# Kernel optimization log

Hardware: AMD Instinct MI355X
Metric: run time of the kernel (lower is better)

## Reference

```python
import jax, jax.numpy as jnp
import numpy as np
import math

H, B, T = 4, 32, 1000
EPROJS, DUNITS, DK, DV = 1024, 1024, 512, 512
ACONV_CHANS, ACONV_FILTS = 100, 100
FILTS = [ACONV_FILTS * (h + 1) // H for h in range(H)]  # 25, 50, 75, 100


def setup_inputs() -> dict:
    key = jax.random.key(0)
    ks = jax.random.split(key, 16)
    s = 0.02  # small init to keep tanh unsaturated
    ap = jax.random.uniform(ks[3], (H, B, T), dtype=jnp.float32)
    ap = ap / ap.sum(-1, keepdims=True)  # previous attention weights (rows sum to 1)
    inp = {
        "enc_hs_pad": jax.random.normal(ks[0], (B, T, EPROJS), dtype=jnp.float32),
        "enc_hs_len": jnp.full((B,), T, dtype=jnp.int32),
        "dec_z": jax.random.normal(ks[1], (B, DUNITS), dtype=jnp.float32),
        "att_prev": ap,
        "Wq": jax.random.normal(ks[4], (H, DUNITS, DK), dtype=jnp.float32) * s,
        "bq": jnp.zeros((H, DK), dtype=jnp.float32),
        "Wk": jax.random.normal(ks[5], (H, EPROJS, DK), dtype=jnp.float32) * s,
        "Wv": jax.random.normal(ks[6], (H, EPROJS, DV), dtype=jnp.float32) * s,
        "g_w": jax.random.normal(ks[7], (H, DK), dtype=jnp.float32) * s,
        "g_b": jnp.zeros((H,), dtype=jnp.float32),
        "Watt": jax.random.normal(ks[8], (H, ACONV_CHANS, DK), dtype=jnp.float32) * s,
        "Wo": jax.random.normal(ks[9], (H * DV, EPROJS), dtype=jnp.float32) * s,
    }
    for h in range(H):
        inp[f"conv_w{h}"] = jax.random.normal(ks[10 + h], (ACONV_CHANS, 1, 2 * FILTS[h] + 1), dtype=jnp.float32) * s
    return inp


def _conv1d(x, w, f):
    # x: [B, T], w: [C, 1, K]; SAME padding like torch Conv2d(padding=(0, f)) -> [B, C, T]
    return jax.lax.conv_general_dilated(x[:, None, :], w, (1,), [(f, f)],
                                        dimension_numbers=("NCH", "OIH", "NCH"))


def reference(enc_hs_pad, enc_hs_len, dec_z, att_prev, Wq, bq, Wk, Wv, g_w, g_b,
              Watt, Wo, conv_w0, conv_w1, conv_w2, conv_w3):
    scaling = 1.0 / math.sqrt(DK)
    conv_ws = [conv_w0, conv_w1, conv_w2, conv_w3]
    # per-head K/V projections of encoder states: [H, B, T, dk/dv]
    k = jnp.einsum('btd,hde->hbte', enc_hs_pad, Wk)
    v = jnp.einsum('btd,hde->hbte', enc_hs_pad, Wv)
    # per-head query projection: [H, B, dk]
    q = jnp.einsum('bd,hde->hbe', dec_z, Wq) + bq[:, None, :]
    # location features: per-head conv (different filter widths) then linear -> [H, B, T, dk]
    att_conv = jnp.stack([_conv1d(att_prev[h], conv_ws[h], FILTS[h]).transpose(0, 2, 1)
                          for h in range(H)])  # [H, B, T, C]
    att_conv = jnp.einsum('hbtc,hce->hbte', att_conv, Watt)
    # energies via gvec: [H, B, T]
    e = jnp.einsum('hbte,he->hbt', jnp.tanh(k + att_conv + q[:, :, None, :]), g_w) + g_b[:, None, None]
    w = jax.nn.softmax(scaling * e, axis=-1)  # no length masking, as in the original
    # weighted sums per head, concatenated head-major: [B, H*dv]
    c = jnp.einsum('hbte,hbt->bhe', v, w).reshape(B, H * DV)
    out = c @ Wo  # [B, eprojs]
    return out, w
```

## Files before the change

### kernel.cpp

```cpp
#include <hip/hip_runtime.h>
#include <hip/hip_bf16.h>
#include <math.h>

#define Hh 4
#define Bb 32
#define Tt 1000
#define TP 1024
#define EPROJS_ 1024
#define DUNITS_ 1024
#define DKd 512
#define DVd 512
#define CC 100
#define KPAD 256
#define SCALING 0.04419417382415922f

typedef __attribute__((ext_vector_type(8))) short short8;
typedef __attribute__((ext_vector_type(4))) float floatx4;

__device__ __forceinline__ void async16(const void* g, void* l) {
    __builtin_amdgcn_global_load_lds(
        (const __attribute__((address_space(1))) unsigned int*)g,
        (__attribute__((address_space(3))) unsigned int*)l, 16, 0, 0);
}

__device__ __forceinline__ float fast_tanh(float x) {
    float xc = fminf(fmaxf(x, -10.f), 10.f);
    float t = __expf(2.f * xc);
    return (t - 1.f) * __builtin_amdgcn_rcpf(t + 1.f);
}

__global__ __launch_bounds__(256) void enc_cvt_kernel(
    const float* __restrict__ enc, unsigned short* __restrict__ enc16)
{
    int t = blockIdx.x, b = blockIdx.y;
    int d = threadIdx.x * 4;
    float4 v = *(const float4*)(enc + ((size_t)(b * Tt + t)) * EPROJS_ + d);
    union { __hip_bfloat162 h2[2]; uint2 u; } u;
    u.h2[0] = __float22bfloat162_rn(make_float2(v.x, v.y));
    u.h2[1] = __float22bfloat162_rn(make_float2(v.z, v.w));
    *(uint2*)(enc16 + ((size_t)(b * TP + t)) * EPROJS_ + d) = u.u;
}

__global__ __launch_bounds__(256) void wkt_kernel(
    const float* __restrict__ Wk, unsigned short* __restrict__ Wkt)
{
    int et = blockIdx.x;
    int dt = blockIdx.y;
    int h  = blockIdx.z;
    __shared__ float tile[64][65];
    int tid = threadIdx.x;
    int r = tid >> 4, c4 = tid & 15;
    const float* src = Wk + ((size_t)(h * DUNITS_ + dt * 64)) * DKd + et * 64;
#pragma unroll
    for (int rr = 0; rr < 4; ++rr) {
        int row = r + rr * 16;
        *(float4*)&tile[row][c4 * 4] = *(const float4*)(src + (size_t)row * DKd + c4 * 4);
    }
    __syncthreads();
    unsigned short* dst = Wkt + ((size_t)(h * DKd + et * 64)) * EPROJS_ + dt * 64;
#pragma unroll
    for (int rr = 0; rr < 4; ++rr) {
        int el = r + rr * 16;
        union { __hip_bfloat162 h2[2]; uint2 u; } u;
        u.h2[0] = __float22bfloat162_rn(make_float2(tile[c4 * 4 + 0][el], tile[c4 * 4 + 1][el]));
        u.h2[1] = __float22bfloat162_rn(make_float2(tile[c4 * 4 + 2][el], tile[c4 * 4 + 3][el]));
        *(uint2*)(dst + (size_t)el * EPROJS_ + c4 * 4) = u.u;
    }
}

__global__ __launch_bounds__(256) void ww_kernel(
    const float* __restrict__ w0, const float* __restrict__ w1,
    const float* __restrict__ w2, const float* __restrict__ w3,
    const float* __restrict__ Watt, __hip_bfloat16* __restrict__ WWt)
{
    int k = blockIdx.x;
    int h = blockIdx.y;
    int f = 25 * (h + 1), Kh = 2 * f + 1;
    const float* cw = (h == 0) ? w0 : (h == 1) ? w1 : (h == 2) ? w2 : w3;
    int e = threadIdx.x;
    float acc0 = 0.f, acc1 = 0.f;
    if (k < Kh) {
        for (int c = 0; c < CC; ++c) {
            float wv = cw[c * Kh + k];
            acc0 += wv * Watt[(h * CC + c) * DKd + e];
            acc1 += wv * Watt[(h * CC + c) * DKd + e + 256];
        }
    }
    WWt[((size_t)(h * DKd + e)) * KPAD + k] = __float2bfloat16(acc0);
    WWt[((size_t)(h * DKd + e + 256)) * KPAD + k] = __float2bfloat16(acc1);
}

__global__ __launch_bounds__(256) void q_kernel(
    const float* __restrict__ dec_z, const float* __restrict__ Wq,
    float* __restrict__ q_buf)
{
    int et = blockIdx.x, kc = blockIdx.y, h = blockIdx.z;
    int d0 = kc * 64;
    __shared__ float zs[32][64];
    int tid = threadIdx.x;
    {
        int b = tid >> 3, dc = (tid & 7) * 8;
        const float* p = dec_z + (size_t)b * DUNITS_ + d0 + dc;
        *(float4*)&zs[b][dc] = *(const float4*)p;
        *(float4*)&zs[b][dc + 4] = *(const float4*)(p + 4);
    }
    __syncthreads();
    int e = et * 128 + (tid & 127);
    int dl0 = (tid >> 7) * 32;
    float wq[32];
#pragma unroll
    for (int dl = 0; dl < 32; ++dl)
        wq[dl] = Wq[((size_t)(h * DUNITS_ + d0 + dl0 + dl)) * DKd + e];
#pragma unroll
    for (int b = 0; b < 32; ++b) {
        float s = 0.f;
#pragma unroll
        for (int dl = 0; dl < 32; ++dl) s += zs[b][dl0 + dl] * wq[dl];
        atomicAdd(&q_buf[(h * Bb + b) * DKd + e], s);
    }
}

__global__ __launch_bounds__(512, 2) void e_kernel(
    const unsigned short* __restrict__ enc16, const unsigned short* __restrict__ Wkt,
    const float* __restrict__ att_prev, const __hip_bfloat16* __restrict__ WWt,
    const float* __restrict__ q_buf, const float* __restrict__ bq,
    const float* __restrict__ g_w, float* __restrict__ e_buf)
{
    const int lin = blockIdx.x;
    const int xcd = lin & 7, pos = lin >> 3;
    const int b = (pos >> 5) * 8 + xcd;
    const int rem = pos & 31;
    const int h = rem >> 3;
    const int by = (rem >> 1) & 3;
    const int bx = rem & 1;
    const int t0 = by * 256, e0 = bx * 256;
    const int tid = threadIdx.x;
    const int lane = tid & 63, w = tid >> 6;
    const int wr = w >> 2, wc = w & 3;
    const int m = lane & 15, quad = lane >> 4;
    const int srow = tid >> 3;
    const int ko = (((tid & 7) ^ (srow & 7))) * 8;
    const int sw = m & 7;

    __shared__ __align__(16) short As[2][256 * 64];
    __shared__ __align__(16) short Bs[2][256 * 64];

    floatx4 acc[8][4];
#pragma unroll
    for (int i = 0; i < 8; ++i)
#pragma unroll
        for (int j = 0; j < 4; ++j) acc[i][j] = (floatx4){0.f, 0.f, 0.f, 0.f};

    const unsigned short* WkB = Wkt + ((size_t)(h * DKd + e0)) * EPROJS_;
    const unsigned short* encB = enc16 + ((size_t)(b * TP + t0)) * EPROJS_;

    auto stage1 = [&](int chunk, int bi) {
        const int d0 = chunk * 64;
        char* ad = (char*)As[bi] + (tid & ~63) * 16;
        char* bd = (char*)Bs[bi] + (tid & ~63) * 16;
#pragma unroll
        for (int it = 0; it < 4; ++it) {
            int r2 = it * 64 + srow;
            async16(encB + (size_t)r2 * EPROJS_ + d0 + ko, ad + it * 8192);
            async16(WkB + (size_t)r2 * EPROJS_ + d0 + ko, bd + it * 8192);
        }
    };

    stage1(0, 0);
    for (int ch = 0; ch < 16; ++ch) {
        const int cur = ch & 1;
        if (ch < 15) {
            stage1(ch + 1, cur ^ 1);
            asm volatile("s_waitcnt vmcnt(8)" ::: "memory");
        } else {
            asm volatile("s_waitcnt vmcnt(0)" ::: "memory");
        }
        __builtin_amdgcn_sched_barrier(0);
        __builtin_amdgcn_s_barrier();
        __builtin_amdgcn_sched_barrier(0);
#pragma unroll
        for (int ph = 0; ph < 4; ++ph) {
            const int ks = ph >> 1, mh = ph & 1;
            const int col = (((ks << 2) + quad) ^ sw) * 8;
            short8 af[4], bf[4];
#pragma unroll
            for (int i = 0; i < 4; ++i)
                af[i] = *(const short8*)&As[cur][(wr * 128 + mh * 64 + i * 16 + m) * 64 + col];
#pragma unroll
            for (int j = 0; j < 4; ++j)
                bf[j] = *(const short8*)&Bs[cur][(wc * 64 + j * 16 + m) * 64 + col];
            __builtin_amdgcn_sched_barrier(0);
            __builtin_amdgcn_s_barrier();
            asm volatile("s_waitcnt lgkmcnt(0)" ::: "memory");
            __builtin_amdgcn_sched_barrier(0);
            __builtin_amdgcn_s_setprio(1);
#pragma unroll
            for (int i = 0; i < 4; ++i)
#pragma unroll
                for (int j = 0; j < 4; ++j)
                    acc[mh * 4 + i][j] = __builtin_amdgcn_mfma_f32_16x16x32_bf16(
                        af[i], bf[j], acc[mh * 4 + i][j], 0, 0, 0);
            __builtin_amdgcn_s_setprio(0);
            __builtin_amdgcn_sched_barrier(0);
            __builtin_amdgcn_s_barrier();
        }
    }

    const int f = 25 * (h + 1);
    const int Kh = 2 * f + 1;
    const int nch2 = (Kh + 63) >> 6;
    const float* ab = att_prev + (size_t)(h * Bb + b) * Tt;
    const __hip_bfloat16* WWB = WWt + ((size_t)(h * DKd + e0)) * KPAD;
    char* BsDst0 = (char*)Bs[0] + (tid & ~63) * 16;
    for (int ch = 0; ch < nch2; ++ch) {
        int k0 = ch * 64;
        int ar = tid >> 1, half = tid & 1;
        int sbase = t0 + ar - f + k0 + half * 32;
        float v[32];
#pragma unroll
        for (int j2 = 0; j2 < 32; ++j2) {
            int s = sbase + j2;
            v[j2] = (s >= 0 && s < Tt) ? ab[s] : 0.f;
        }
        __syncthreads();
#pragma unroll
        for (int it = 0; it < 4; ++it) {
            int r2 = it * 64 + srow;
            async16(WWB + (size_t)r2 * KPAD + k0 + ko, BsDst0 + it * 8192);
        }
        union { short8 s[4]; __hip_bfloat162 hh[16]; } u;
#pragma unroll
        for (int j2 = 0; j2 < 16; ++j2)
            u.hh[j2] = __float22bfloat162_rn(make_float2(v[2 * j2], v[2 * j2 + 1]));
#pragma unroll
        for (int jj = 0; jj < 4; ++jj) {
            int phys = (half * 4 + jj) ^ (ar & 7);
            *(short8*)&As[0][ar * 64 + phys * 8] = u.s[jj];
        }
        __syncthreads();
#pragma unroll
        for (int ks = 0; ks < 2; ++ks) {
            short8 af[8], bf[4];
#pragma unroll
            for (int i = 0; i < 8; ++i)
                af[i] = *(const short8*)&As[0][(wr * 128 + i * 16 + m) * 64 + (((ks << 2) + quad) ^ sw) * 8];
#pragma unroll
            for (int j = 0; j < 4; ++j)
                bf[j] = *(const short8*)&Bs[0][(wc * 64 + j * 16 + m) * 64 + (((ks << 2) + quad) ^ sw) * 8];
            __builtin_amdgcn_s_setprio(1);
#pragma unroll
            for (int i = 0; i < 8; ++i)
#pragma unroll
                for (int j = 0; j < 4; ++j)
                    acc[i][j] = __builtin_amdgcn_mfma_f32_16x16x32_bf16(
                        af[i], bf[j], acc[i][j], 0, 0, 0);
            __builtin_amdgcn_s_setprio(0);
        }
    }

    const float* qrow = q_buf + (size_t)(h * Bb + b) * DKd;
    const float* bqrow = bq + h * DKd;
    const float* gwrow = g_w + h * DKd;
    float qv[4], gw[4];
#pragma unroll
    for (int j = 0; j < 4; ++j) {
        int e = e0 + wc * 64 + j * 16 + m;
        qv[j] = qrow[e] + bqrow[e];
        gw[j] = gwrow[e];
    }
    float* erow = e_buf + (size_t)(h * Bb + b) * Tt;
#pragma unroll
    for (int i = 0; i < 8; ++i) {
#pragma unroll
        for (int reg = 0; reg < 4; ++reg) {
            float s = 0.f;
#pragma unroll
            for (int j = 0; j < 4; ++j)
                s += fast_tanh(acc[i][j][reg] + qv[j]) * gw[j];
            s += __shfl_xor(s, 1);
            s += __shfl_xor(s, 2);
            s += __shfl_xor(s, 4);
            s += __shfl_xor(s, 8);
            int t = t0 + wr * 128 + i * 16 + quad * 4 + reg;
            if (m == 0 && t < Tt)
                atomicAdd(&erow[t], s);
        }
    }
}

__global__ __launch_bounds__(256) void softmax_kernel(
    const float* __restrict__ e_buf, float* __restrict__ wout)
{
    int rowid = blockIdx.x;
    const float* x = e_buf + rowid * Tt;
    float* y = wout + rowid * Tt;
    int tid = threadIdx.x;
    float v[4];
    float mx = -1e30f;
#pragma unroll
    for (int k = 0; k < 4; ++k) {
        int t = tid + k * 256;
        v[k] = (t < Tt) ? x[t] * SCALING : -1e30f;
        mx = fmaxf(mx, v[k]);
    }
    for (int off = 32; off >= 1; off >>= 1) mx = fmaxf(mx, __shfl_xor(mx, off));
    __shared__ float sm[4];
    __shared__ float ss[4];
    int wave = tid >> 6;
    if ((tid & 63) == 0) sm[wave] = mx;
    __syncthreads();
    mx = fmaxf(fmaxf(sm[0], sm[1]), fmaxf(sm[2], sm[3]));
    float s = 0.f;
#pragma unroll
    for (int k = 0; k < 4; ++k) {
        int t = tid + k * 256;
        v[k] = (t < Tt) ? __expf(v[k] - mx) : 0.f;
        s += v[k];
    }
    for (int off = 32; off >= 1; off >>= 1) s += __shfl_xor(s, off);
    if ((tid & 63) == 0) ss[wave] = s;
    __syncthreads();
    s = ss[0] + ss[1] + ss[2] + ss[3];
    float inv = 1.0f / s;
#pragma unroll
    for (int k = 0; k < 4; ++k) {
        int t = tid + k * 256;
        if (t < Tt) y[t] = v[k] * inv;
    }
}

__global__ __launch_bounds__(256) void ctx_kernel(
    const float* __restrict__ wout, const unsigned short* __restrict__ enc16,
    float* __restrict__ ctx)
{
    int dch = blockIdx.x;
    int b = blockIdx.y;
    int tq = blockIdx.z;
    int t0 = tq * 250;
    int tid = threadIdx.x;
    __shared__ float wl[4][252];
    __shared__ float red[8 * 4 * 128];
    for (int i = tid; i < 1000; i += 256) {
        int h = i / 250, tl = i - h * 250;
        wl[h][tl] = wout[(h * Bb + b) * Tt + t0 + tl];
    }
    __syncthreads();
    int g = tid >> 5, c = tid & 31;
    int d0 = dch * 128;
    float4 a[4];
#pragma unroll
    for (int h = 0; h < 4; ++h) a[h] = make_float4(0.f, 0.f, 0.f, 0.f);
    const unsigned short* encB = enc16 + (size_t)b * TP * EPROJS_ + d0 + c * 4;
    for (int t = t0 + g; t < t0 + 250; t += 8) {
        uint2 raw = *(const uint2*)(encB + (size_t)t * EPROJS_);
        float x0 = __uint_as_float(raw.x << 16);
        float x1 = __uint_as_float(raw.x & 0xffff0000u);
        float x2 = __uint_as_float(raw.y << 16);
        float x3 = __uint_as_float(raw.y & 0xffff0000u);
#pragma unroll
        for (int h = 0; h < 4; ++h) {
            float wv = wl[h][t - t0];
            a[h].x += wv * x0; a[h].y += wv * x1;
            a[h].z += wv * x2; a[h].w += wv * x3;
        }
    }
#pragma unroll
    for (int h = 0; h < 4; ++h)
        *(float4*)&red[((g * 4 + h) << 7) + c * 4] = a[h];
    __syncthreads();
    for (int i = tid; i < 512; i += 256) {
        int h = i >> 7, dd = i & 127;
        float ssum = 0.f;
#pragma unroll
        for (int g2 = 0; g2 < 8; ++g2) ssum += red[((g2 * 4 + h) << 7) + dd];
        atomicAdd(&ctx[(h * Bb + b) * EPROJS_ + d0 + dd], ssum);
    }
}

__global__ __launch_bounds__(256) void c_kernel(
    const float* __restrict__ ctx, const float* __restrict__ Wv,
    float* __restrict__ c_buf)
{
    int et = blockIdx.x, kc = blockIdx.y, h = blockIdx.z;
    int d0 = kc * 64;
    __shared__ float zs[32][64];
    int tid = threadIdx.x;
    {
        int b = tid >> 3, dc = (tid & 7) * 8;
        const float* p = ctx + ((size_t)(h * Bb + b)) * EPROJS_ + d0 + dc;
        *(float4*)&zs[b][dc] = *(const float4*)p;
        *(float4*)&zs[b][dc + 4] = *(const float4*)(p + 4);
    }
    __syncthreads();
    int e = et * 128 + (tid & 127);
    int dl0 = (tid >> 7) * 32;
    float wv[32];
#pragma unroll
    for (int dl = 0; dl < 32; ++dl)
        wv[dl] = Wv[((size_t)(h * EPROJS_ + d0 + dl0 + dl)) * DVd + e];
#pragma unroll
    for (int b = 0; b < 32; ++b) {
        float s = 0.f;
#pragma unroll
        for (int dl = 0; dl < 32; ++dl) s += zs[b][dl0 + dl] * wv[dl];
        atomicAdd(&c_buf[(h * Bb + b) * DVd + e], s);
    }
}

__global__ __launch_bounds__(256) void out_kernel(
    const float* __restrict__ c_buf, const float* __restrict__ Wo,
    float* __restrict__ outp)
{
    int ot = blockIdx.x;
    int kc = blockIdx.y;
    int k0 = kc * 64, o0 = ot * 128;
    __shared__ float cs[32][64];
    int tid = threadIdx.x;
    {
        int b = tid >> 3, k8 = (tid & 7) * 8;
        int h = k0 >> 9;
        const float* p = c_buf + ((size_t)(h * Bb + b)) * DVd + (k0 & 511) + k8;
        *(float4*)&cs[b][k8] = *(const float4*)p;
        *(float4*)&cs[b][k8 + 4] = *(const float4*)(p + 4);
    }
    __syncthreads();
    int o = o0 + (tid & 127);
    int kl0 = (tid >> 7) * 32;
    float wo[32];
#pragma unroll
    for (int kl = 0; kl < 32; ++kl)
        wo[kl] = Wo[((size_t)(k0 + kl0 + kl)) * EPROJS_ + o];
#pragma unroll
    for (int b = 0; b < 32; ++b) {
        float s = 0.f;
#pragma unroll
        for (int kl = 0; kl < 32; ++kl) s += cs[b][kl0 + kl] * wo[kl];
        atomicAdd(&outp[b * EPROJS_ + o], s);
    }
}

extern "C" void kernel_launch(void* const* d_in, const int* in_sizes, int n_in,
                              void* d_out, int out_size, void* d_ws, size_t ws_size,
                              hipStream_t stream) {
    const float* enc     = (const float*)d_in[0];
    const float* dec_z   = (const float*)d_in[2];
    const float* att_prev= (const float*)d_in[3];
    const float* Wq      = (const float*)d_in[4];
    const float* bq      = (const float*)d_in[5];
    const float* Wk      = (const float*)d_in[6];
    const float* Wv      = (const float*)d_in[7];
    const float* g_w     = (const float*)d_in[8];
    const float* Watt    = (const float*)d_in[10];
    const float* Wo      = (const float*)d_in[11];
    const float* cw0     = (const float*)d_in[12];
    const float* cw1     = (const float*)d_in[13];
    const float* cw2     = (const float*)d_in[14];
    const float* cw3     = (const float*)d_in[15];

    float* ws    = (float*)d_ws;
    float* q_buf = ws;
    float* e_buf = ws + 65536;
    float* c_buf = ws + 193536;
    float* ctx   = ws + 259072;
    unsigned short* enc16 = (unsigned short*)(ws + 390144);
    unsigned short* Wkt   = (unsigned short*)(ws + 17167360);
    __hip_bfloat16* WWt   = (__hip_bfloat16*)(ws + 18215936);
    float* outp  = (float*)d_out;
    float* wout  = outp + 32768;

    hipMemsetAsync(ws, 0, (size_t)390144 * sizeof(float), stream);
    hipMemsetAsync(d_out, 0, (size_t)32768 * sizeof(float), stream);

    enc_cvt_kernel<<<dim3(Tt, Bb), 256, 0, stream>>>(enc, enc16);
    wkt_kernel<<<dim3(8, 16, 4), 256, 0, stream>>>(Wk, Wkt);
    ww_kernel<<<dim3(KPAD, 4), 256, 0, stream>>>(cw0, cw1, cw2, cw3, Watt, WWt);
    q_kernel<<<dim3(4, 16, 4), 256, 0, stream>>>(dec_z, Wq, q_buf);
    e_kernel<<<1024, 512, 0, stream>>>(enc16, Wkt, att_prev, WWt,
                                       q_buf, bq, g_w, e_buf);
    softmax_kernel<<<128, 256, 0, stream>>>(e_buf, wout);
    ctx_kernel<<<dim3(8, 32, 4), 256, 0, stream>>>(wout, enc16, ctx);
    c_kernel<<<dim3(4, 16, 4), 256, 0, stream>>>(ctx, Wv, c_buf);
    out_kernel<<<dim3(8, 32), 256, 0, stream>>>(c_buf, Wo, outp);
}
```

Measured before the change: 543.7 us.

## Merge prep kernels into one launch and interleave async loads across MFMA phases

Folds the four preprocessing kernels (enc bf16 conversion, Wk transpose, conv-Watt fold, query projection) into one prep_kernel whose block ranges pick the task, saving launch overhead and letting small tasks run alongside the large conversion. In the e_kernel main GEMM loop, the next chunk's global-to-LDS async loads are now issued one quarter per MFMA phase, with a single vmcnt(0) wait at the end of each chunk, instead of all at once ahead of the compute. B fragments are also loaded once per k-step rather than per phase. The encoder conversion now uses a grid-stride loop over fewer blocks, and the finer load interleaving could add stalls if the final wait isn't hidden.

```diff
diff --git a/kernel.cpp b/kernel.cpp
--- a/kernel.cpp
+++ b/kernel.cpp
@@ -29,94 +29,92 @@
     return (t - 1.f) * __builtin_amdgcn_rcpf(t + 1.f);
 }
 
-__global__ __launch_bounds__(256) void enc_cvt_kernel(
-    const float* __restrict__ enc, unsigned short* __restrict__ enc16)
-{
-    int t = blockIdx.x, b = blockIdx.y;
-    int d = threadIdx.x * 4;
-    float4 v = *(const float4*)(enc + ((size_t)(b * Tt + t)) * EPROJS_ + d);
-    union { __hip_bfloat162 h2[2]; uint2 u; } u;
-    u.h2[0] = __float22bfloat162_rn(make_float2(v.x, v.y));
-    u.h2[1] = __float22bfloat162_rn(make_float2(v.z, v.w));
-    *(uint2*)(enc16 + ((size_t)(b * TP + t)) * EPROJS_ + d) = u.u;
-}
-
-__global__ __launch_bounds__(256) void wkt_kernel(
-    const float* __restrict__ Wk, unsigned short* __restrict__ Wkt)
-{
-    int et = blockIdx.x;
-    int dt = blockIdx.y;
-    int h  = blockIdx.z;
-    __shared__ float tile[64][65];
-    int tid = threadIdx.x;
-    int r = tid >> 4, c4 = tid & 15;
-    const float* src = Wk + ((size_t)(h * DUNITS_ + dt * 64)) * DKd + et * 64;
-#pragma unroll
-    for (int rr = 0; rr < 4; ++rr) {
-        int row = r + rr * 16;
-        *(float4*)&tile[row][c4 * 4] = *(const float4*)(src + (size_t)row * DKd + c4 * 4);
-    }
-    __syncthreads();
-    unsigned short* dst = Wkt + ((size_t)(h * DKd + et * 64)) * EPROJS_ + dt * 64;
-#pragma unroll
-    for (int rr = 0; rr < 4; ++rr) {
-        int el = r + rr * 16;
-        union { __hip_bfloat162 h2[2]; uint2 u; } u;
-        u.h2[0] = __float22bfloat162_rn(make_float2(tile[c4 * 4 + 0][el], tile[c4 * 4 + 1][el]));
-        u.h2[1] = __float22bfloat162_rn(make_float2(tile[c4 * 4 + 2][el], tile[c4 * 4 + 3][el]));
-        *(uint2*)(dst + (size_t)el * EPROJS_ + c4 * 4) = u.u;
-    }
-}
-
-__global__ __launch_bounds__(256) void ww_kernel(
+__global__ __launch_bounds__(256) void prep_kernel(
+    const float* __restrict__ Wk, unsigned short* __restrict__ Wkt,
     const float* __restrict__ w0, const float* __restrict__ w1,
     const float* __restrict__ w2, const float* __restrict__ w3,
-    const float* __restrict__ Watt, __hip_bfloat16* __restrict__ WWt)
-{
-    int k = blockIdx.x;
-    int h = blockIdx.y;
-    int f = 25 * (h + 1), Kh = 2 * f + 1;
-    const float* cw = (h == 0) ? w0 : (h == 1) ? w1 : (h == 2) ? w2 : w3;
-    int e = threadIdx.x;
-    float acc0 = 0.f, acc1 = 0.f;
-    if (k < Kh) {
-        for (int c = 0; c < CC; ++c) {
-            float wv = cw[c * Kh + k];
-            acc0 += wv * Watt[(h * CC + c) * DKd + e];
-            acc1 += wv * Watt[(h * CC + c) * DKd + e + 256];
-        }
-    }
-    WWt[((size_t)(h * DKd + e)) * KPAD + k] = __float2bfloat16(acc0);
-    WWt[((size_t)(h * DKd + e + 256)) * KPAD + k] = __float2bfloat16(acc1);
-}
-
-__global__ __launch_bounds__(256) void q_kernel(
+    const float* __restrict__ Watt, __hip_bfloat16* __restrict__ WWt,
     const float* __restrict__ dec_z, const float* __restrict__ Wq,
-    float* __restrict__ q_buf)
-{
-    int et = blockIdx.x, kc = blockIdx.y, h = blockIdx.z;
-    int d0 = kc * 64;
-    __shared__ float zs[32][64];
-    int tid = threadIdx.x;
-    {
-        int b = tid >> 3, dc = (tid & 7) * 8;
-        const float* p = dec_z + (size_t)b * DUNITS_ + d0 + dc;
-        *(float4*)&zs[b][dc] = *(const float4*)p;
-        *(float4*)&zs[b][dc + 4] = *(const float4*)(p + 4);
-    }
-    __syncthreads();
-    int e = et * 128 + (tid & 127);
-    int dl0 = (tid >> 7) * 32;
-    float wq[32];
-#pragma unroll
-    for (int dl = 0; dl < 32; ++dl)
-        wq[dl] = Wq[((size_t)(h * DUNITS_ + d0 + dl0 + dl)) * DKd + e];
-#pragma unroll
-    for (int b = 0; b < 32; ++b) {
-        float s = 0.f;
-#pragma unroll
-        for (int dl = 0; dl < 32; ++dl) s += zs[b][dl0 + dl] * wq[dl];
-        atomicAdd(&q_buf[(h * Bb + b) * DKd + e], s);
+    float* __restrict__ q_buf,
+    const float* __restrict__ enc, unsigned short* __restrict__ enc16)
+{
+    __shared__ float shbuf[64 * 65];
+    const int bid = blockIdx.x;
+    const int tid = threadIdx.x;
+    if (bid < 512) {
+        int et = bid & 7, dt = (bid >> 3) & 15, h = bid >> 7;
+        float (*tile)[65] = (float(*)[65])shbuf;
+        int r = tid >> 4, c4 = tid & 15;
+        const float* src = Wk + ((size_t)(h * DUNITS_ + dt * 64)) * DKd + et * 64;
+#pragma unroll
+        for (int rr = 0; rr < 4; ++rr) {
+            int row = r + rr * 16;
+            *(float4*)&tile[row][c4 * 4] = *(const float4*)(src + (size_t)row * DKd + c4 * 4);
+        }
+        __syncthreads();
+        unsigned short* dst = Wkt + ((size_t)(h * DKd + et * 64)) * EPROJS_ + dt * 64;
+#pragma unroll
+        for (int rr = 0; rr < 4; ++rr) {
+            int el = r + rr * 16;
+            union { __hip_bfloat162 h2[2]; uint2 u; } u;
+            u.h2[0] = __float22bfloat162_rn(make_float2(tile[c4 * 4 + 0][el], tile[c4 * 4 + 1][el]));
+            u.h2[1] = __float22bfloat162_rn(make_float2(tile[c4 * 4 + 2][el], tile[c4 * 4 + 3][el]));
+            *(uint2*)(dst + (size_t)el * EPROJS_ + c4 * 4) = u.u;
+        }
+    } else if (bid < 1536) {
+        int b2 = bid - 512;
+        int k = b2 & 255, h = b2 >> 8;
+        int f = 25 * (h + 1), Kh = 2 * f + 1;
+        const float* cw = (h == 0) ? w0 : (h == 1) ? w1 : (h == 2) ? w2 : w3;
+        int e = tid;
+        float acc0 = 0.f, acc1 = 0.f;
+        if (k < Kh) {
+            for (int c = 0; c < CC; ++c) {
+                float wv = cw[c * Kh + k];
+                acc0 += wv * Watt[(h * CC + c) * DKd + e];
+                acc1 += wv * Watt[(h * CC + c) * DKd + e + 256];
+            }
+        }
+        WWt[((size_t)(h * DKd + e)) * KPAD + k] = __float2bfloat16(acc0);
+        WWt[((size_t)(h * DKd + e + 256)) * KPAD + k] = __float2bfloat16(acc1);
+    } else if (bid < 1792) {
+        int b3 = bid - 1536;
+        int et = b3 & 3, kc = (b3 >> 2) & 15, h = b3 >> 6;
+        int d0 = kc * 64;
+        float (*zs)[64] = (float(*)[64])shbuf;
+        {
+            int b = tid >> 3, dc = (tid & 7) * 8;
+            const float* p = dec_z + (size_t)b * DUNITS_ + d0 + dc;
+            *(float4*)&zs[b][dc] = *(const float4*)p;
+            *(float4*)&zs[b][dc + 4] = *(const float4*)(p + 4);
+        }
+        __syncthreads();
+        int e = et * 128 + (tid & 127);
+        int dl0 = (tid >> 7) * 32;
+        float wq[32];
+#pragma unroll
+        for (int dl = 0; dl < 32; ++dl)
+            wq[dl] = Wq[((size_t)(h * DUNITS_ + d0 + dl0 + dl)) * DKd + e];
+#pragma unroll
+        for (int b = 0; b < 32; ++b) {
+            float s = 0.f;
+#pragma unroll
+            for (int dl = 0; dl < 32; ++dl) s += zs[b][dl0 + dl] * wq[dl];
+            atomicAdd(&q_buf[(h * Bb + b) * DKd + e], s);
+        }
+    } else {
+        const int total = Bb * Tt * (EPROJS_ / 4);
+        const int nblk = 2048;
+        for (int idx = (bid - 1792) * 256 + tid; idx < total; idx += nblk * 256) {
+            int d4 = idx & 255;
+            int bt = idx >> 8;
+            int b = bt / Tt, t = bt - b * Tt;
+            float4 v = *(const float4*)(enc + (size_t)idx * 4);
+            union { __hip_bfloat162 h2[2]; uint2 u; } u;
+            u.h2[0] = __float22bfloat162_rn(make_float2(v.x, v.y));
+            u.h2[1] = __float22bfloat162_rn(make_float2(v.z, v.w));
+            *(uint2*)(enc16 + ((size_t)(b * TP + t)) * EPROJS_ + d4 * 4) = u.u;
+        }
     }
 }
 
@@ -154,41 +152,37 @@
     const unsigned short* WkB = Wkt + ((size_t)(h * DKd + e0)) * EPROJS_;
     const unsigned short* encB = enc16 + ((size_t)(b * TP + t0)) * EPROJS_;
 
-    auto stage1 = [&](int chunk, int bi) {
+    auto stage2 = [&](int chunk, int bi, int it) {
         const int d0 = chunk * 64;
         char* ad = (char*)As[bi] + (tid & ~63) * 16;
         char* bd = (char*)Bs[bi] + (tid & ~63) * 16;
-#pragma unroll
-        for (int it = 0; it < 4; ++it) {
-            int r2 = it * 64 + srow;
-            async16(encB + (size_t)r2 * EPROJS_ + d0 + ko, ad + it * 8192);
-            async16(WkB + (size_t)r2 * EPROJS_ + d0 + ko, bd + it * 8192);
-        }
+        int r2 = it * 64 + srow;
+        async16(encB + (size_t)r2 * EPROJS_ + d0 + ko, ad + it * 8192);
+        async16(WkB + (size_t)r2 * EPROJS_ + d0 + ko, bd + it * 8192);
     };
 
-    stage1(0, 0);
+#pragma unroll
+    for (int it = 0; it < 4; ++it) stage2(0, 0, it);
+    asm volatile("s_waitcnt vmcnt(0)" ::: "memory");
+    __builtin_amdgcn_s_barrier();
+
     for (int ch = 0; ch < 16; ++ch) {
         const int cur = ch & 1;
-        if (ch < 15) {
-            stage1(ch + 1, cur ^ 1);
-            asm volatile("s_waitcnt vmcnt(8)" ::: "memory");
-        } else {
-            asm volatile("s_waitcnt vmcnt(0)" ::: "memory");
-        }
-        __builtin_amdgcn_sched_barrier(0);
-        __builtin_amdgcn_s_barrier();
-        __builtin_amdgcn_sched_barrier(0);
+        short8 bf[4];
 #pragma unroll
         for (int ph = 0; ph < 4; ++ph) {
-            const int ks = ph >> 1, mh = ph & 1;
+            const int ks = ph >> 1, ih = ph & 1;
             const int col = (((ks << 2) + quad) ^ sw) * 8;
-            short8 af[4], bf[4];
+            short8 af[4];
 #pragma unroll
             for (int i = 0; i < 4; ++i)
-                af[i] = *(const short8*)&As[cur][(wr * 128 + mh * 64 + i * 16 + m) * 64 + col];
-#pragma unroll
-            for (int j = 0; j < 4; ++j)
-                bf[j] = *(const short8*)&Bs[cur][(wc * 64 + j * 16 + m) * 64 + col];
+                af[i] = *(const short8*)&As[cur][(wr * 128 + ih * 64 + i * 16 + m) * 64 + col];
+            if (ih == 0) {
+#pragma unroll
+                for (int j = 0; j < 4; ++j)
+                    bf[j] = *(const short8*)&Bs[cur][(wc * 64 + j * 16 + m) * 64 + col];
+            }
+            if (ch < 15) stage2(ch + 1, cur ^ 1, ph);
             __builtin_amdgcn_sched_barrier(0);
             __builtin_amdgcn_s_barrier();
             asm volatile("s_waitcnt lgkmcnt(0)" ::: "memory");
@@ -198,10 +192,12 @@
             for (int i = 0; i < 4; ++i)
 #pragma unroll
                 for (int j = 0; j < 4; ++j)
-                    acc[mh * 4 + i][j] = __builtin_amdgcn_mfma_f32_16x16x32_bf16(
-                        af[i], bf[j], acc[mh * 4 + i][j], 0, 0, 0);
+                    acc[ih * 4 + i][j] = __builtin_amdgcn_mfma_f32_16x16x32_bf16(
+                        af[i], bf[j], acc[ih * 4 + i][j], 0, 0, 0);
             __builtin_amdgcn_s_setprio(0);
             __builtin_amdgcn_sched_barrier(0);
+            if (ph == 3 && ch < 15)
+                asm volatile("s_waitcnt vmcnt(0)" ::: "memory");
             __builtin_amdgcn_s_barrier();
         }
     }
@@ -240,20 +236,20 @@
         __syncthreads();
 #pragma unroll
         for (int ks = 0; ks < 2; ++ks) {
-            short8 af[8], bf[4];
+            short8 af[8], bf2[4];
 #pragma unroll
             for (int i = 0; i < 8; ++i)
                 af[i] = *(const short8*)&As[0][(wr * 128 + i * 16 + m) * 64 + (((ks << 2) + quad) ^ sw) * 8];
 #pragma unroll
             for (int j = 0; j < 4; ++j)
-                bf[j] = *(const short8*)&Bs[0][(wc * 64 + j * 16 + m) * 64 + (((ks << 2) + quad) ^ sw) * 8];
+                bf2[j] = *(const short8*)&Bs[0][(wc * 64 + j * 16 + m) * 64 + (((ks << 2) + quad) ^ sw) * 8];
             __builtin_amdgcn_s_setprio(1);
 #pragma unroll
             for (int i = 0; i < 8; ++i)
 #pragma unroll
                 for (int j = 0; j < 4; ++j)
                     acc[i][j] = __builtin_amdgcn_mfma_f32_16x16x32_bf16(
-                        af[i], bf[j], acc[i][j], 0, 0, 0);
+                        af[i], bf2[j], acc[i][j], 0, 0, 0);
             __builtin_amdgcn_s_setprio(0);
         }
     }
@@ -471,10 +467,8 @@
     hipMemsetAsync(ws, 0, (size_t)390144 * sizeof(float), stream);
     hipMemsetAsync(d_out, 0, (size_t)32768 * sizeof(float), stream);
 
-    enc_cvt_kernel<<<dim3(Tt, Bb), 256, 0, stream>>>(enc, enc16);
-    wkt_kernel<<<dim3(8, 16, 4), 256, 0, stream>>>(Wk, Wkt);
-    ww_kernel<<<dim3(KPAD, 4), 256, 0, stream>>>(cw0, cw1, cw2, cw3, Watt, WWt);
-    q_kernel<<<dim3(4, 16, 4), 256, 0, stream>>>(dec_z, Wq, q_buf);
+    prep_kernel<<<3840, 256, 0, stream>>>(Wk, Wkt, cw0, cw1, cw2, cw3, Watt, WWt,
+                                          dec_z, Wq, q_buf, enc, enc16);
     e_kernel<<<1024, 512, 0, stream>>>(enc16, Wkt, att_prev, WWt,
                                        q_buf, bq, g_w, e_buf);
     softmax_kernel<<<128, 256, 0, stream>>>(e_buf, wout);
```

After: 497.6 us. 8.5% less time.
